# Kernel optimization log

Hardware: AMD Instinct MI355X
Metric: run time of the kernel (lower is better)

The kernel has to match this reference:

```python
import jax, jax.numpy as jnp
import numpy as np

# Pool2d config (init_kwargs): 3x3 max pool, stride 2, symmetric pad 1, dilation 1
K = 3
STRIDE = 2
PAD = 1  # (left, right, top, bottom) all equal
DIL = 1
FILL = 0.0  # padding_fill_value


def setup_inputs() -> dict:
    key = jax.random.key(0)
    X = jax.random.normal(key, (32, 192, 224, 224), dtype=jnp.float32)  # NCHW
    return {"X": X}


def reference(X):
    # F.pad with constant padding_fill_value, then sliding-window max over KxK
    # (dilated) patches with the given stride -- same math as unfold + max
    # reduce over the patch axis, but without materializing K*K patches.
    Xp = jnp.pad(X, ((0, 0), (0, 0), (PAD, PAD), (PAD, PAD)), constant_values=FILL)
    Y = jax.lax.reduce_window(
        Xp,
        -jnp.inf,
        jax.lax.max,
        window_dimensions=(1, 1, K, K),
        window_strides=(1, 1, STRIDE, STRIDE),
        padding='VALID',
        window_dilation=(1, 1, DIL, DIL),
    )  # [N, C, H_out, W_out] = [32, 192, 112, 112]
    return Y
```

## Files before the change

### kernel.cpp

```cpp
#include <hip/hip_runtime.h>
#include <math.h>


namespace {
constexpr int H = 224;
constexpr int W = 224;
constexpr int HO = 112;
constexpr int WO = 112;
constexpr int QPR = WO / 4;
constexpr int NROWS = 32 * 192 * HO;
constexpr int TOTAL_QUADS = NROWS * QPR;
}

__global__ __launch_bounds__(256) void pool3x3s2_kernel(
    const float* __restrict__ X, float* __restrict__ Y) {
  const int stride = gridDim.x * blockDim.x;
  for (int idx = blockIdx.x * blockDim.x + threadIdx.x; idx < TOTAL_QUADS;
       idx += stride) {
    const int q   = idx % QPR;
    const int row = idx / QPR;
    const int oy  = row % HO;
    const int nc  = row / HO;

    const float* __restrict__ img = X + (size_t)nc * (H * W);
    const int iy0 = 2 * oy - 1;
    const int ixs = 8 * q;

    float m0 = -INFINITY, m1 = -INFINITY, m2 = -INFINITY, m3 = -INFINITY;

#pragma unroll
    for (int dy = 0; dy < 3; ++dy) {
      const int iy = iy0 + dy;
      float a, b0, b1, b2, b3, b4, b5, b6, b7;
      if (0 <= iy && iy < H) {
        const float* __restrict__ r = img + iy * W;
        a = (ixs > 0) ? r[ixs - 1] : 0.0f;
        const float4 v0 = *reinterpret_cast<const float4*>(r + ixs);
        const float4 v1 = *reinterpret_cast<const float4*>(r + ixs + 4);
        b0 = v0.x; b1 = v0.y; b2 = v0.z; b3 = v0.w;
        b4 = v1.x; b5 = v1.y; b6 = v1.z; b7 = v1.w;
      } else {
        a = b0 = b1 = b2 = b3 = b4 = b5 = b6 = b7 = 0.0f;
      }
      m0 = fmaxf(m0, fmaxf(a,  fmaxf(b0, b1)));
      m1 = fmaxf(m1, fmaxf(b1, fmaxf(b2, b3)));
      m2 = fmaxf(m2, fmaxf(b3, fmaxf(b4, b5)));
      m3 = fmaxf(m3, fmaxf(b5, fmaxf(b6, b7)));
    }

    float4 o;
    o.x = m0; o.y = m1; o.z = m2; o.w = m3;
    *reinterpret_cast<float4*>(Y + (size_t)row * WO + 4 * q) = o;
  }
}

extern "C" void kernel_launch(void* const* d_in, const int* in_sizes, int n_in,
                              void* d_out, int out_size, void* d_ws, size_t ws_size,
                              hipStream_t stream) {
  const float* X = (const float*)d_in[0];
  float* Y = (float*)d_out;
  pool3x3s2_kernel<<<2048, 256, 0, stream>>>(X, Y);
}
```

Measured before the change: 309.4 us.

## Stage input row bands in LDS per block and use nontemporal output stores

Each block now handles one quarter (28 output rows) of a single image channel. It first copies the 57 input rows that quarter needs into shared memory with vectorized loads, zero-filling the top padding row, then computes the 3x3 stride-2 max from LDS. Outputs are written with nontemporal stores. The aim is to read each input row from global memory roughly once, without relying on cache for the row overlap between neighbouring output rows, and to keep output writes from polluting the cache. The trade-off is about 51KB of LDS per block, which limits occupancy, a barrier between the load and compute phases, and one redundant halo row per quarter.

```diff
diff --git a/kernel.cpp b/kernel.cpp
--- a/kernel.cpp
+++ b/kernel.cpp
@@ -7,50 +7,63 @@
 constexpr int W = 224;
 constexpr int HO = 112;
 constexpr int WO = 112;
-constexpr int QPR = WO / 4;
-constexpr int NROWS = 32 * 192 * HO;
-constexpr int TOTAL_QUADS = NROWS * QPR;
+constexpr int NC = 32 * 192;
+constexpr int OROWS = 28;
+constexpr int IROWS = 57;
+constexpr int F4PR = W / 4;
+constexpr int NF4 = IROWS * F4PR;
+constexpr int LDSF = IROWS * W;
+constexpr int NQUAD = OROWS * (WO / 4);
+
+typedef float v4f __attribute__((ext_vector_type(4)));
 }
 
-__global__ __launch_bounds__(256) void pool3x3s2_kernel(
+__global__ __launch_bounds__(256) void pool3x3s2_lds(
     const float* __restrict__ X, float* __restrict__ Y) {
-  const int stride = gridDim.x * blockDim.x;
-  for (int idx = blockIdx.x * blockDim.x + threadIdx.x; idx < TOTAL_QUADS;
-       idx += stride) {
-    const int q   = idx % QPR;
-    const int row = idx / QPR;
-    const int oy  = row % HO;
-    const int nc  = row / HO;
+  __shared__ float lds[LDSF];
+  const int b   = blockIdx.x;
+  const int Q   = b & 3;
+  const int nc  = b >> 2;
+  const int tid = threadIdx.x;
 
-    const float* __restrict__ img = X + (size_t)nc * (H * W);
-    const int iy0 = 2 * oy - 1;
-    const int ixs = 8 * q;
+  const float* __restrict__ img = X + (size_t)nc * (H * W);
+  const int ibase = 56 * Q - 1;
+
+  for (int f = tid; f < NF4; f += 256) {
+    const int r = f / F4PR;
+    const int c = f - r * F4PR;
+    const int iy = ibase + r;
+    v4f v;
+    if (iy >= 0) {
+      v = *reinterpret_cast<const v4f*>(img + iy * W + 4 * c);
+    } else {
+      v = 0.0f;
+    }
+    *reinterpret_cast<v4f*>(&lds[4 * f]) = v;
+  }
+  __syncthreads();
+
+  float* __restrict__ outq = Y + (size_t)nc * (HO * WO) + Q * OROWS * WO;
+  for (int hq = tid; hq < NQUAD; hq += 256) {
+    const int oy = hq / 28;
+    const int q  = hq - oy * 28;
 
     float m0 = -INFINITY, m1 = -INFINITY, m2 = -INFINITY, m3 = -INFINITY;
-
 #pragma unroll
-    for (int dy = 0; dy < 3; ++dy) {
-      const int iy = iy0 + dy;
-      float a, b0, b1, b2, b3, b4, b5, b6, b7;
-      if (0 <= iy && iy < H) {
-        const float* __restrict__ r = img + iy * W;
-        a = (ixs > 0) ? r[ixs - 1] : 0.0f;
-        const float4 v0 = *reinterpret_cast<const float4*>(r + ixs);
-        const float4 v1 = *reinterpret_cast<const float4*>(r + ixs + 4);
-        b0 = v0.x; b1 = v0.y; b2 = v0.z; b3 = v0.w;
-        b4 = v1.x; b5 = v1.y; b6 = v1.z; b7 = v1.w;
-      } else {
-        a = b0 = b1 = b2 = b3 = b4 = b5 = b6 = b7 = 0.0f;
-      }
-      m0 = fmaxf(m0, fmaxf(a,  fmaxf(b0, b1)));
-      m1 = fmaxf(m1, fmaxf(b1, fmaxf(b2, b3)));
-      m2 = fmaxf(m2, fmaxf(b3, fmaxf(b4, b5)));
-      m3 = fmaxf(m3, fmaxf(b5, fmaxf(b6, b7)));
+    for (int d = 0; d < 3; ++d) {
+      const float* __restrict__ lr = &lds[(2 * oy + d) * W + 8 * q];
+      const float a = (q > 0) ? lr[-1] : 0.0f;
+      const v4f v0 = *reinterpret_cast<const v4f*>(lr);
+      const v4f v1 = *reinterpret_cast<const v4f*>(lr + 4);
+      m0 = fmaxf(m0, fmaxf(fmaxf(a,    v0.x), v0.y));
+      m1 = fmaxf(m1, fmaxf(fmaxf(v0.y, v0.z), v0.w));
+      m2 = fmaxf(m2, fmaxf(fmaxf(v0.w, v1.x), v1.y));
+      m3 = fmaxf(m3, fmaxf(fmaxf(v1.y, v1.z), v1.w));
     }
-
-    float4 o;
+    v4f o;
     o.x = m0; o.y = m1; o.z = m2; o.w = m3;
-    *reinterpret_cast<float4*>(Y + (size_t)row * WO + 4 * q) = o;
+    __builtin_nontemporal_store(
+        o, reinterpret_cast<v4f*>(outq + oy * WO + 4 * q));
   }
 }
 
@@ -59,5 +72,5 @@
                               hipStream_t stream) {
   const float* X = (const float*)d_in[0];
   float* Y = (float*)d_out;
-  pool3x3s2_kernel<<<2048, 256, 0, stream>>>(X, Y);
+  pool3x3s2_lds<<<NC * 4, 256, 0, stream>>>(X, Y);
 }
```

Measured after the change: 341.0 us. 10.2% more time.
